# Kernel optimization log

Measured on AMD Instinct MI355X. Metric: run time of the kernel, lower is better.

The kernel has to match this reference:

```python
import jax, jax.numpy as jnp
import numpy as np

N_TREES, N_LEAVES, PATH_LEN, N_NODES, D, B = 10, 16, 5, 31, 256, 4096


def _local_paths():
    # root-to-leaf paths of a full binary tree, depth 4: 31 nodes, 16 leaves, path len 5
    return np.array([[0, 1 + l // 8, 3 + l // 4, 7 + l // 2, 15 + l]
                     for l in range(N_LEAVES)], np.int32)


def setup_inputs() -> dict:
    key = jax.random.key(0)
    k1, k2, k3, k4, k5, k6 = jax.random.split(key, 6)
    # one activated leaf per tree -> multi-hot cross_features (B, N_TREES*N_LEAVES)
    leaf = jax.random.randint(k1, (B, N_TREES), 0, N_LEAVES)
    cross = jnp.zeros((B, N_TREES, N_LEAVES), jnp.float32)
    cross = cross.at[jnp.arange(B)[:, None], jnp.arange(N_TREES)[None, :], leaf].set(1.0)
    cross_features = cross.reshape(B, N_TREES * N_LEAVES)
    # learned params: node embedding table + single-layer LSTM (torch init scale 1/sqrt(D))
    emb = jax.random.normal(k2, (N_TREES * N_NODES, D), jnp.float32) * 0.02
    s = 1.0 / np.sqrt(D)
    W_ih = jax.random.uniform(k3, (4 * D, D), jnp.float32, -s, s)
    W_hh = jax.random.uniform(k4, (4 * D, D), jnp.float32, -s, s)
    b_ih = jax.random.uniform(k5, (4 * D,), jnp.float32, -s, s)
    b_hh = jax.random.uniform(k6, (4 * D,), jnp.float32, -s, s)
    return {"cross_features": cross_features, "emb": emb, "W_ih": W_ih,
            "W_hh": W_hh, "b_ih": b_ih, "b_hh": b_hh}


def reference(cross_features, emb, W_ih, W_hh, b_ih, b_hh):
    # global path node ids per (tree, leaf): [T, L, P]
    gpaths = jnp.asarray(_local_paths())[None, :, :] + \
        (jnp.arange(N_TREES, dtype=jnp.int32) * N_NODES)[:, None, None]
    # activated leaf per tree (exactly one hot per 16-leaf block)
    leaf = jnp.argmax(cross_features.reshape(B, N_TREES, N_LEAVES), axis=-1)  # [B, T]
    node_ids = gpaths[jnp.arange(N_TREES)[None, :], leaf]                     # [B, T, P]
    x = emb[node_ids].reshape(B * N_TREES, PATH_LEN, D)                       # packed paths
    # precompute input projections for all steps: [N, P, 4D]
    xg = jnp.einsum('npd,gd->npg', x, W_ih) + (b_ih + b_hh)

    def step(carry, xt):
        h, c = carry
        g = xt + h @ W_hh.T
        i, f, gg, o = jnp.split(g, 4, axis=-1)  # torch gate order: i, f, g, o
        c = jax.nn.sigmoid(f) * c + jax.nn.sigmoid(i) * jnp.tanh(gg)
        h = jax.nn.sigmoid(o) * jnp.tanh(c)
        return (h, c), None

    n = B * N_TREES
    h0 = jnp.zeros((n, D), x.dtype)
    (h, _), _ = jax.lax.scan(step, (h0, h0), jnp.swapaxes(xg, 0, 1))
    return h.reshape(B, N_TREES, D)
```

## Files before the change

### kernel.cpp

```cpp
#include <hip/hip_runtime.h>

#define NT 10
#define NL 16
#define NN 31
#define DD 256
#define G4 1024
#define NNODES (NT*NN)
#define NPATH (NT*NL)
#define NB 4096

__device__ unsigned g_tf[3][NT][32];

__device__ __forceinline__ float sigf(float x)   { return 1.0f / (1.0f + __expf(-x)); }
__device__ __forceinline__ float tanh_f(float x) { return 2.0f / (1.0f + __expf(-2.0f*x)) - 1.0f; }

__device__ __forceinline__ void co_store(float* p, float v) {
    union { float f; unsigned u; } c; c.f = v;
    __hip_atomic_store((unsigned*)p, c.u, __ATOMIC_RELAXED, __HIP_MEMORY_SCOPE_AGENT);
}

__global__ __launch_bounds__(256) void k_nodeproj(
    const float* __restrict__ emb, const float* __restrict__ Wih,
    const float* __restrict__ bih, const float* __restrict__ bhh,
    float* __restrict__ xg)
{
    __shared__ float smem[20 * 260 + 20 * 4 * 64];
    float4* es4 = (float4*)smem;
    float*  ps  = smem + 20 * 260;

    const int tid = threadIdx.x;
    const int nt  = blockIdx.x & 15;
    const int mt  = blockIdx.x >> 4;
    const int kq  = tid >> 6;
    const int w   = tid & 63;

    const float4* W4 = (const float4*)Wih + (size_t)(nt * 64 + w) * 64 + kq * 16;
    float4 wr[16];
    #pragma unroll
    for (int j = 0; j < 16; ++j) wr[j] = W4[j];

    const float4* emb4 = (const float4*)emb;
    #pragma unroll
    for (int r = 0; r < 5; ++r) {
        int idx = tid + 256 * r;
        int m = idx >> 6, q = idx & 63;
        int n = mt * 20 + m;
        es4[m * 65 + q] = (n < NNODES) ? emb4[(size_t)n * 64 + q]
                                       : make_float4(0.f, 0.f, 0.f, 0.f);
    }
    __syncthreads();

    float acc[20];
    #pragma unroll
    for (int m = 0; m < 20; ++m) acc[m] = 0.f;
    #pragma unroll
    for (int j = 0; j < 16; ++j) {
        float4 wv = wr[j];
        #pragma unroll
        for (int m = 0; m < 20; ++m) {
            float4 h = es4[m * 65 + kq * 16 + j];
            acc[m] = fmaf(wv.x, h.x, fmaf(wv.y, h.y,
                     fmaf(wv.z, h.z, fmaf(wv.w, h.w, acc[m]))));
        }
    }
    #pragma unroll
    for (int m = 0; m < 20; ++m) ps[(m * 4 + kq) * 64 + w] = acc[m];
    __syncthreads();

    const int nl   = tid & 63;
    const int msub = tid >> 6;
    const int j    = nt * 64 + nl;
    const float bsum = bih[j] + bhh[j];
    #pragma unroll
    for (int r = 0; r < 5; ++r) {
        int m = msub * 5 + r;
        int n = mt * 20 + m;
        float s = ps[(m * 4 + 0) * 64 + nl] + ps[(m * 4 + 1) * 64 + nl]
                + ps[(m * 4 + 2) * 64 + nl] + ps[(m * 4 + 3) * 64 + nl];
        if (n < NNODES) xg[(size_t)n * G4 + j] = s + bsum;
    }
}

__global__ __launch_bounds__(256) void k_treesteps(
    const float* __restrict__ xg, const float* __restrict__ Whh,
    float* __restrict__ h1g, float* __restrict__ h2g,
    float* __restrict__ h3g, float* __restrict__ h4g)
{
    __shared__ float hs[8 * DD];
    __shared__ float ps[8 * DD];
    __shared__ float cbuf[2][8 * 16];

    const int tid  = threadIdx.x;
    const int t    = blockIdx.x >> 4;
    const int dt   = blockIdx.x & 15;
    const int kq   = tid >> 6;
    const int w    = tid & 63;
    const int gate = w >> 4;
    const int col  = w & 15;

    const unsigned base = __hip_atomic_load(&g_tf[2][t][0],
        __ATOMIC_RELAXED, __HIP_MEMORY_SCOPE_AGENT);

    const float4* W4 = (const float4*)Whh
        + (size_t)(gate * DD + dt * 16 + col) * 64 + kq * 16;
    float4 wreg[16];
    #pragma unroll
    for (int j = 0; j < 16; ++j) wreg[j] = W4[j];

    float xnv[4][4];
    #pragma unroll
    for (int s = 1; s <= 4; ++s) {
        xnv[s-1][0] = 0.f; xnv[s-1][1] = 0.f;
        xnv[s-1][2] = 0.f; xnv[s-1][3] = 0.f;
        if (tid < (32 << (s - 1))) {
            int node = (1 << s) - 1 + (tid >> 4);
            const float* xn = xg + (size_t)(t * NN + node) * G4 + dt * 16 + (tid & 15);
            xnv[s-1][0] = xn[0];
            xnv[s-1][1] = xn[256];
            xnv[s-1][2] = xn[512];
            xnv[s-1][3] = xn[768];
        }
    }

    {
        const float* xr = xg + (size_t)(t * NN) * G4;
        float r_i = xr[tid], r_g = xr[512 + tid], r_o = xr[768 + tid];
        float c0 = sigf(r_i) * tanh_f(r_g);
        float h0 = sigf(r_o) * tanh_f(c0);
        hs[tid] = h0;
        if ((tid >> 4) == dt) cbuf[0][tid & 15] = c0;
    }
    __syncthreads();

    float* hout[3] = { h1g, h2g, h3g };
    const float* hin[3] = { h1g, h2g, h3g };

    #pragma unroll
    for (int s = 1; s <= 4; ++s) {
        const int L = 1 << (s - 1);

        if (s > 1) {
            if (tid < 64) {
                const unsigned tgt = base + 16u;
                while (__hip_atomic_load(&g_tf[s - 2][t][0],
                        __ATOMIC_RELAXED, __HIP_MEMORY_SCOPE_AGENT) < tgt)
                    __builtin_amdgcn_s_sleep(2);
            }
            __syncthreads();
            const unsigned long long* src =
                (const unsigned long long*)(hin[s - 2] + (size_t)t * L * DD);
            unsigned long long raw[4];
            #pragma unroll
            for (int r = 0; r < L / 2; ++r)
                raw[r] = __hip_atomic_load(src + tid + 256 * r,
                    __ATOMIC_RELAXED, __HIP_MEMORY_SCOPE_AGENT);
            float2* hs2 = (float2*)hs;
            #pragma unroll
            for (int r = 0; r < L / 2; ++r) {
                union { unsigned long long u; float2 f; } cv; cv.u = raw[r];
                hs2[tid + 256 * r] = cv.f;
            }
            __syncthreads();
        }

        const float4* hs4 = (const float4*)hs;
        float acc[8];
        #pragma unroll
        for (int p = 0; p < 8; ++p) acc[p] = 0.f;
        #pragma unroll
        for (int j = 0; j < 16; ++j) {
            float4 wv = wreg[j];
            #pragma unroll
            for (int p = 0; p < L; ++p) {
                float4 h = hs4[p * 64 + kq * 16 + j];
                acc[p] = fmaf(wv.x, h.x, fmaf(wv.y, h.y,
                         fmaf(wv.z, h.z, fmaf(wv.w, h.w, acc[p]))));
            }
        }
        #pragma unroll
        for (int p = 0; p < L; ++p) ps[p * DD + kq * 64 + w] = acc[p];
        __syncthreads();

        if (tid < 32 * L) {
            const int p  = tid >> 5;
            const int c2 = tid & 15;
            const int q  = tid >> 4;
            float g0 = 0.f, g1 = 0.f, g2 = 0.f, g3 = 0.f;
            #pragma unroll
            for (int k = 0; k < 4; ++k) {
                const float* pp = ps + p * DD + k * 64;
                g0 += pp[ 0 + c2]; g1 += pp[16 + c2];
                g2 += pp[32 + c2]; g3 += pp[48 + c2];
            }
            float gi = g0 + xnv[s - 1][0];
            float gf = g1 + xnv[s - 1][1];
            float gg = g2 + xnv[s - 1][2];
            float go = g3 + xnv[s - 1][3];
            float cin = cbuf[(s - 1) & 1][p * 16 + c2];
            float cn  = sigf(gf) * cin + sigf(gi) * tanh_f(gg);
            float hn  = sigf(go) * tanh_f(cn);
            if (s < 4) {
                cbuf[s & 1][q * 16 + c2] = cn;
                co_store(hout[s - 1] + (size_t)(t * 2 * L + q) * DD
                                     + dt * 16 + c2, hn);
            } else {
                h4g[(size_t)(t * NL + q) * DD + dt * 16 + c2] = hn;
            }
        }

        if (s < 4) {
            __syncthreads();
            if (tid == 0)
                __hip_atomic_fetch_add(&g_tf[s - 1][t][0], 1u,
                    __ATOMIC_RELAXED, __HIP_MEMORY_SCOPE_AGENT);
        }
    }
}

__global__ __launch_bounds__(256) void k_scatter(
    const float* __restrict__ cross, const float* __restrict__ htab,
    float* __restrict__ out)
{
    const int tid  = threadIdx.x;
    const int wave = tid >> 6;
    const int lane = tid & 63;
    const int r = blockIdx.x * 4 + wave;
    const int b = r / NT;
    const int t = r - b * NT;

    float v = 0.f;
    if (lane < NL) v = cross[(size_t)b * (NT * NL) + t * NL + lane];
    unsigned long long m = __ballot(v > 0.5f);
    int leaf = m ? (int)__builtin_ctzll(m) : 0;
    int p = t * NL + leaf;

    const float4* h4 = (const float4*)htab;
    float4* o4 = (float4*)out;
    o4[(size_t)r * 64 + lane] = h4[(size_t)p * 64 + lane];
}

extern "C" void kernel_launch(void* const* d_in, const int* in_sizes, int n_in,
                              void* d_out, int out_size, void* d_ws, size_t ws_size,
                              hipStream_t stream)
{
    const float* cross = (const float*)d_in[0];
    const float* emb   = (const float*)d_in[1];
    const float* Wih   = (const float*)d_in[2];
    const float* Whh   = (const float*)d_in[3];
    const float* bih   = (const float*)d_in[4];
    const float* bhh   = (const float*)d_in[5];
    float* out = (float*)d_out;

    float* ws = (float*)d_ws;
    float* xg = ws;
    float* h1 = xg + (size_t)NNODES * G4;
    float* h2 = h1 + 20 * DD;
    float* h3 = h2 + 40 * DD;
    float* h4 = h3 + 80 * DD;

    hipLaunchKernelGGL(k_nodeproj, dim3(256), dim3(256), 0, stream,
                       emb, Wih, bih, bhh, xg);
    hipLaunchKernelGGL(k_treesteps, dim3(160), dim3(256), 0, stream,
                       xg, Whh, h1, h2, h3, h4);
    hipLaunchKernelGGL(k_scatter, dim3(10240), dim3(256), 0, stream,
                       cross, h4, out);
}
```

Baseline: 111.8 us.

## Regroup tree-step LSTM into 4 blocks per tree and batch scatter rows per block

The recurrent tree-step kernel now uses 40 blocks of 512 threads, one per (tree, quarter of hidden dim), instead of 160 blocks of 256 threads. Each thread holds two W_hh rows in registers, and cross-block sync counters become per-quarter flags polled with a wave vote. This cuts the number of blocks that must synchronize through global memory at each step. The scatter kernel now stages 64 rows of cross features in shared memory per block and copies 64 output rows per block, instead of one row per wave. The cost is doubled register pressure in the step kernel and fewer CUs in use.

```diff
diff --git a/kernel.cpp b/kernel.cpp
--- a/kernel.cpp
+++ b/kernel.cpp
@@ -81,54 +81,72 @@
     }
 }
 
-__global__ __launch_bounds__(256) void k_treesteps(
+__global__ __launch_bounds__(512) void k_treesteps(
     const float* __restrict__ xg, const float* __restrict__ Whh,
     float* __restrict__ h1g, float* __restrict__ h2g,
     float* __restrict__ h3g, float* __restrict__ h4g)
 {
     __shared__ float hs[8 * DD];
-    __shared__ float ps[8 * DD];
-    __shared__ float cbuf[2][8 * 16];
-
-    const int tid  = threadIdx.x;
-    const int t    = blockIdx.x >> 4;
-    const int dt   = blockIdx.x & 15;
-    const int kq   = tid >> 6;
-    const int w    = tid & 63;
-    const int gate = w >> 4;
-    const int col  = w & 15;
-
-    const unsigned base = __hip_atomic_load(&g_tf[2][t][0],
-        __ATOMIC_RELAXED, __HIP_MEMORY_SCOPE_AGENT);
-
-    const float4* W4 = (const float4*)Whh
-        + (size_t)(gate * DD + dt * 16 + col) * 64 + kq * 16;
-    float4 wreg[16];
-    #pragma unroll
-    for (int j = 0; j < 16; ++j) wreg[j] = W4[j];
-
-    float xnv[4][4];
+    __shared__ float ps[8 * 4 * DD];
+    __shared__ float cbuf[2][8 * 64];
+
+    const int tid = threadIdx.x;
+    const int t   = blockIdx.x >> 2;
+    const int d4  = blockIdx.x & 3;
+    const int kq  = tid >> 7;
+    const int u   = tid & 127;
+    const int c   = tid & 63;
+    const int q0  = tid >> 6;
+
+    unsigned mybase = 0;
+    if (tid < 4)
+        mybase = __hip_atomic_load(&g_tf[2][t][tid],
+            __ATOMIC_RELAXED, __HIP_MEMORY_SCOPE_AGENT);
+
+    float4 wreg[2][16];
+    #pragma unroll
+    for (int rq = 0; rq < 2; ++rq) {
+        int r    = u + 128 * rq;
+        int grow = (r >> 6) * 256 + d4 * 64 + (r & 63);
+        const float4* Wp = (const float4*)Whh + (size_t)grow * 64 + kq * 16;
+        #pragma unroll
+        for (int j = 0; j < 16; ++j) wreg[rq][j] = Wp[j];
+    }
+
+    float xnv[4][2][4];
     #pragma unroll
     for (int s = 1; s <= 4; ++s) {
-        xnv[s-1][0] = 0.f; xnv[s-1][1] = 0.f;
-        xnv[s-1][2] = 0.f; xnv[s-1][3] = 0.f;
-        if (tid < (32 << (s - 1))) {
-            int node = (1 << s) - 1 + (tid >> 4);
-            const float* xn = xg + (size_t)(t * NN + node) * G4 + dt * 16 + (tid & 15);
-            xnv[s-1][0] = xn[0];
-            xnv[s-1][1] = xn[256];
-            xnv[s-1][2] = xn[512];
-            xnv[s-1][3] = xn[768];
-        }
-    }
-
-    {
+        #pragma unroll
+        for (int h = 0; h < 2; ++h) {
+            xnv[s-1][h][0] = xnv[s-1][h][1] = 0.f;
+            xnv[s-1][h][2] = xnv[s-1][h][3] = 0.f;
+        }
+        int nact = (s == 4) ? 512 : (64 << s);
+        if (tid < nact) {
+            int node = (1 << s) - 1 + q0;
+            const float* xn = xg + (size_t)(t * NN + node) * G4 + d4 * 64 + c;
+            xnv[s-1][0][0] = xn[0];
+            xnv[s-1][0][1] = xn[256];
+            xnv[s-1][0][2] = xn[512];
+            xnv[s-1][0][3] = xn[768];
+        }
+        if (s == 4) {
+            int node = 15 + q0 + 8;
+            const float* xn = xg + (size_t)(t * NN + node) * G4 + d4 * 64 + c;
+            xnv[3][1][0] = xn[0];
+            xnv[3][1][1] = xn[256];
+            xnv[3][1][2] = xn[512];
+            xnv[3][1][3] = xn[768];
+        }
+    }
+
+    if (tid < 256) {
         const float* xr = xg + (size_t)(t * NN) * G4;
         float r_i = xr[tid], r_g = xr[512 + tid], r_o = xr[768 + tid];
         float c0 = sigf(r_i) * tanh_f(r_g);
-        float h0 = sigf(r_o) * tanh_f(c0);
-        hs[tid] = h0;
-        if ((tid >> 4) == dt) cbuf[0][tid & 15] = c0;
+        hs[tid]  = sigf(r_o) * tanh_f(c0);
+        int lc = tid - d4 * 64;
+        if (lc >= 0 && lc < 64) cbuf[0][lc] = c0;
     }
     __syncthreads();
 
@@ -141,77 +159,97 @@
 
         if (s > 1) {
             if (tid < 64) {
-                const unsigned tgt = base + 16u;
-                while (__hip_atomic_load(&g_tf[s - 2][t][0],
-                        __ATOMIC_RELAXED, __HIP_MEMORY_SCOPE_AGENT) < tgt)
-                    __builtin_amdgcn_s_sleep(2);
+                for (;;) {
+                    bool ok = true;
+                    if (tid < 4)
+                        ok = __hip_atomic_load(&g_tf[s - 2][t][tid],
+                                __ATOMIC_RELAXED, __HIP_MEMORY_SCOPE_AGENT)
+                             > mybase;
+                    if (__all(ok)) break;
+                    __builtin_amdgcn_s_sleep(1);
+                }
             }
             __syncthreads();
             const unsigned long long* src =
                 (const unsigned long long*)(hin[s - 2] + (size_t)t * L * DD);
-            unsigned long long raw[4];
-            #pragma unroll
-            for (int r = 0; r < L / 2; ++r)
-                raw[r] = __hip_atomic_load(src + tid + 256 * r,
+            const int n64 = L * 128;
+            unsigned long long raw0 = 0, raw1 = 0;
+            if (tid < n64)
+                raw0 = __hip_atomic_load(src + tid,
+                    __ATOMIC_RELAXED, __HIP_MEMORY_SCOPE_AGENT);
+            if (512 + tid < n64)
+                raw1 = __hip_atomic_load(src + 512 + tid,
                     __ATOMIC_RELAXED, __HIP_MEMORY_SCOPE_AGENT);
             float2* hs2 = (float2*)hs;
-            #pragma unroll
-            for (int r = 0; r < L / 2; ++r) {
-                union { unsigned long long u; float2 f; } cv; cv.u = raw[r];
-                hs2[tid + 256 * r] = cv.f;
+            if (tid < n64) {
+                union { unsigned long long u; float2 f; } cv; cv.u = raw0;
+                hs2[tid] = cv.f;
+            }
+            if (512 + tid < n64) {
+                union { unsigned long long u; float2 f; } cv; cv.u = raw1;
+                hs2[512 + tid] = cv.f;
             }
             __syncthreads();
         }
 
         const float4* hs4 = (const float4*)hs;
-        float acc[8];
-        #pragma unroll
-        for (int p = 0; p < 8; ++p) acc[p] = 0.f;
+        float acc[2][8];
+        #pragma unroll
+        for (int p = 0; p < 8; ++p) { acc[0][p] = 0.f; acc[1][p] = 0.f; }
         #pragma unroll
         for (int j = 0; j < 16; ++j) {
-            float4 wv = wreg[j];
+            float4 w0 = wreg[0][j], w1 = wreg[1][j];
             #pragma unroll
             for (int p = 0; p < L; ++p) {
                 float4 h = hs4[p * 64 + kq * 16 + j];
-                acc[p] = fmaf(wv.x, h.x, fmaf(wv.y, h.y,
-                         fmaf(wv.z, h.z, fmaf(wv.w, h.w, acc[p]))));
-            }
-        }
-        #pragma unroll
-        for (int p = 0; p < L; ++p) ps[p * DD + kq * 64 + w] = acc[p];
+                acc[0][p] = fmaf(w0.x, h.x, fmaf(w0.y, h.y,
+                            fmaf(w0.z, h.z, fmaf(w0.w, h.w, acc[0][p]))));
+                acc[1][p] = fmaf(w1.x, h.x, fmaf(w1.y, h.y,
+                            fmaf(w1.z, h.z, fmaf(w1.w, h.w, acc[1][p]))));
+            }
+        }
+        #pragma unroll
+        for (int p = 0; p < L; ++p) {
+            ps[((p << 2) | kq) * 256 + u]       = acc[0][p];
+            ps[((p << 2) | kq) * 256 + u + 128] = acc[1][p];
+        }
         __syncthreads();
 
-        if (tid < 32 * L) {
-            const int p  = tid >> 5;
-            const int c2 = tid & 15;
-            const int q  = tid >> 4;
-            float g0 = 0.f, g1 = 0.f, g2 = 0.f, g3 = 0.f;
-            #pragma unroll
-            for (int k = 0; k < 4; ++k) {
-                const float* pp = ps + p * DD + k * 64;
-                g0 += pp[ 0 + c2]; g1 += pp[16 + c2];
-                g2 += pp[32 + c2]; g3 += pp[48 + c2];
-            }
-            float gi = g0 + xnv[s - 1][0];
-            float gf = g1 + xnv[s - 1][1];
-            float gg = g2 + xnv[s - 1][2];
-            float go = g3 + xnv[s - 1][3];
-            float cin = cbuf[(s - 1) & 1][p * 16 + c2];
-            float cn  = sigf(gf) * cin + sigf(gi) * tanh_f(gg);
-            float hn  = sigf(go) * tanh_f(cn);
-            if (s < 4) {
-                cbuf[s & 1][q * 16 + c2] = cn;
-                co_store(hout[s - 1] + (size_t)(t * 2 * L + q) * DD
-                                     + dt * 16 + c2, hn);
-            } else {
-                h4g[(size_t)(t * NL + q) * DD + dt * 16 + c2] = hn;
+        const int halves = (s == 4) ? 2 : 1;
+        #pragma unroll
+        for (int hh = 0; hh < halves; ++hh) {
+            int q = q0 + 8 * hh;
+            bool act = (hh == 1) || (tid < (64 << s));
+            if (act) {
+                int p = q >> 1;
+                float g0 = 0.f, g1 = 0.f, g2 = 0.f, g3 = 0.f;
+                #pragma unroll
+                for (int k = 0; k < 4; ++k) {
+                    const float* pp = ps + ((p << 2) | k) * 256;
+                    g0 += pp[c]; g1 += pp[64 + c];
+                    g2 += pp[128 + c]; g3 += pp[192 + c];
+                }
+                float gi = g0 + xnv[s - 1][hh][0];
+                float gf = g1 + xnv[s - 1][hh][1];
+                float gg = g2 + xnv[s - 1][hh][2];
+                float go = g3 + xnv[s - 1][hh][3];
+                float cin = cbuf[(s - 1) & 1][p * 64 + c];
+                float cn  = sigf(gf) * cin + sigf(gi) * tanh_f(gg);
+                float hn  = sigf(go) * tanh_f(cn);
+                if (s < 4) {
+                    cbuf[s & 1][q * 64 + c] = cn;
+                    co_store(hout[s - 1] + (size_t)(t * 2 * L + q) * DD
+                                         + d4 * 64 + c, hn);
+                } else {
+                    h4g[(size_t)(t * NL + q) * DD + d4 * 64 + c] = hn;
+                }
             }
         }
 
         if (s < 4) {
             __syncthreads();
             if (tid == 0)
-                __hip_atomic_fetch_add(&g_tf[s - 1][t][0], 1u,
+                __hip_atomic_fetch_add(&g_tf[s - 1][t][d4], 1u,
                     __ATOMIC_RELAXED, __HIP_MEMORY_SCOPE_AGENT);
         }
     }
@@ -221,22 +259,37 @@
     const float* __restrict__ cross, const float* __restrict__ htab,
     float* __restrict__ out)
 {
-    const int tid  = threadIdx.x;
-    const int wave = tid >> 6;
-    const int lane = tid & 63;
-    const int r = blockIdx.x * 4 + wave;
-    const int b = r / NT;
-    const int t = r - b * NT;
-
-    float v = 0.f;
-    if (lane < NL) v = cross[(size_t)b * (NT * NL) + t * NL + lane];
-    unsigned long long m = __ballot(v > 0.5f);
-    int leaf = m ? (int)__builtin_ctzll(m) : 0;
-    int p = t * NL + leaf;
+    __shared__ float cls[1024];
+    __shared__ int   leafs[64];
+    const int tid = threadIdx.x;
+    const size_t r0 = (size_t)blockIdx.x * 64;
+
+    #pragma unroll
+    for (int k = 0; k < 4; ++k)
+        cls[tid + 256 * k] = cross[r0 * 16 + tid + 256 * k];
+    __syncthreads();
+
+    if (tid < 64) {
+        int leaf = 0;
+        #pragma unroll
+        for (int l = 15; l >= 0; --l)
+            if (cls[tid * 16 + l] > 0.5f) leaf = l;
+        int r = (int)(r0 + (size_t)tid);
+        int b = r / NT;
+        int t = r - b * NT;
+        leafs[tid] = t * 16 + leaf;
+    }
+    __syncthreads();
 
     const float4* h4 = (const float4*)htab;
     float4* o4 = (float4*)out;
-    o4[(size_t)r * 64 + lane] = h4[(size_t)p * 64 + lane];
+    const int lane = tid & 63;
+    const int sub  = tid >> 6;
+    #pragma unroll
+    for (int it = 0; it < 16; ++it) {
+        int rr = it * 4 + sub;
+        o4[(r0 + rr) * 64 + lane] = h4[(size_t)leafs[rr] * 64 + lane];
+    }
 }
 
 extern "C" void kernel_launch(void* const* d_in, const int* in_sizes, int n_in,
@@ -260,8 +313,8 @@
 
     hipLaunchKernelGGL(k_nodeproj, dim3(256), dim3(256), 0, stream,
                        emb, Wih, bih, bhh, xg);
-    hipLaunchKernelGGL(k_treesteps, dim3(160), dim3(256), 0, stream,
+    hipLaunchKernelGGL(k_treesteps, dim3(40), dim3(512), 0, stream,
                        xg, Whh, h1, h2, h3, h4);
-    hipLaunchKernelGGL(k_scatter, dim3(10240), dim3(256), 0, stream,
+    hipLaunchKernelGGL(k_scatter, dim3(640), dim3(256), 0, stream,
                        cross, h4, out);
 }
```

Result: slower. 115.8 us (+3.6%).

## Fuse node projection, tree LSTM steps and leaf scatter into one persistent kernel

Applied to the files above, without the earlier changes.

Merges the three launches into a single kernel whose block ranges play producer/consumer roles, synchronised through generation-counted global flags with release/acquire fences. This removes two launch boundaries and lets the LSTM blocks preload Whh while the projection runs, and lets the scatter blocks decode leaves early. The scatter becomes 256 blocks each handling 160 rows with batched loads, instead of 10240 small blocks. It relies on all 672 blocks being co-resident (launch bounds allow 3 per CU), otherwise the spin-waits can deadlock.

```diff
diff --git a/kernel.cpp b/kernel.cpp
--- a/kernel.cpp
+++ b/kernel.cpp
@@ -9,7 +9,10 @@
 #define NPATH (NT*NL)
 #define NB 4096
 
-__device__ unsigned g_tf[3][NT][32];
+__device__ unsigned g_xgf[16];
+__device__ unsigned g_tf[3][NT][16];
+__device__ unsigned g_h4f[NT];
+__device__ unsigned g_sgen[256];
 
 __device__ __forceinline__ float sigf(float x)   { return 1.0f / (1.0f + __expf(-x)); }
 __device__ __forceinline__ float tanh_f(float x) { return 2.0f / (1.0f + __expf(-2.0f*x)) - 1.0f; }
@@ -18,225 +21,306 @@
     union { float f; unsigned u; } c; c.f = v;
     __hip_atomic_store((unsigned*)p, c.u, __ATOMIC_RELAXED, __HIP_MEMORY_SCOPE_AGENT);
 }
-
-__global__ __launch_bounds__(256) void k_nodeproj(
-    const float* __restrict__ emb, const float* __restrict__ Wih,
-    const float* __restrict__ bih, const float* __restrict__ bhh,
-    float* __restrict__ xg)
-{
-    __shared__ float smem[20 * 260 + 20 * 4 * 64];
-    float4* es4 = (float4*)smem;
-    float*  ps  = smem + 20 * 260;
-
-    const int tid = threadIdx.x;
-    const int nt  = blockIdx.x & 15;
-    const int mt  = blockIdx.x >> 4;
-    const int kq  = tid >> 6;
-    const int w   = tid & 63;
-
-    const float4* W4 = (const float4*)Wih + (size_t)(nt * 64 + w) * 64 + kq * 16;
-    float4 wr[16];
-    #pragma unroll
-    for (int j = 0; j < 16; ++j) wr[j] = W4[j];
-
-    const float4* emb4 = (const float4*)emb;
-    #pragma unroll
-    for (int r = 0; r < 5; ++r) {
-        int idx = tid + 256 * r;
-        int m = idx >> 6, q = idx & 63;
-        int n = mt * 20 + m;
-        es4[m * 65 + q] = (n < NNODES) ? emb4[(size_t)n * 64 + q]
-                                       : make_float4(0.f, 0.f, 0.f, 0.f);
-    }
-    __syncthreads();
-
-    float acc[20];
-    #pragma unroll
-    for (int m = 0; m < 20; ++m) acc[m] = 0.f;
-    #pragma unroll
-    for (int j = 0; j < 16; ++j) {
-        float4 wv = wr[j];
-        #pragma unroll
-        for (int m = 0; m < 20; ++m) {
-            float4 h = es4[m * 65 + kq * 16 + j];
-            acc[m] = fmaf(wv.x, h.x, fmaf(wv.y, h.y,
-                     fmaf(wv.z, h.z, fmaf(wv.w, h.w, acc[m]))));
-        }
-    }
-    #pragma unroll
-    for (int m = 0; m < 20; ++m) ps[(m * 4 + kq) * 64 + w] = acc[m];
-    __syncthreads();
-
-    const int nl   = tid & 63;
-    const int msub = tid >> 6;
-    const int j    = nt * 64 + nl;
-    const float bsum = bih[j] + bhh[j];
-    #pragma unroll
-    for (int r = 0; r < 5; ++r) {
-        int m = msub * 5 + r;
-        int n = mt * 20 + m;
-        float s = ps[(m * 4 + 0) * 64 + nl] + ps[(m * 4 + 1) * 64 + nl]
-                + ps[(m * 4 + 2) * 64 + nl] + ps[(m * 4 + 3) * 64 + nl];
-        if (n < NNODES) xg[(size_t)n * G4 + j] = s + bsum;
-    }
-}
-
-__global__ __launch_bounds__(256) void k_treesteps(
-    const float* __restrict__ xg, const float* __restrict__ Whh,
+__device__ __forceinline__ float co_load(const float* p) {
+    union { unsigned u; float f; } c;
+    c.u = __hip_atomic_load((const unsigned*)p, __ATOMIC_RELAXED, __HIP_MEMORY_SCOPE_AGENT);
+    return c.f;
+}
+__device__ __forceinline__ unsigned long long co_load64(const unsigned long long* p) {
+    return __hip_atomic_load(p, __ATOMIC_RELAXED, __HIP_MEMORY_SCOPE_AGENT);
+}
+__device__ __forceinline__ unsigned flag_load(const unsigned* p) {
+    return __hip_atomic_load(p, __ATOMIC_RELAXED, __HIP_MEMORY_SCOPE_AGENT);
+}
+__device__ __forceinline__ void rel_add(unsigned* p) {
+    __hip_atomic_fetch_add(p, 1u, __ATOMIC_RELEASE, __HIP_MEMORY_SCOPE_AGENT);
+}
+__device__ __forceinline__ void acq_fence() {
+    __builtin_amdgcn_fence(__ATOMIC_ACQUIRE, "agent");
+}
+
+__global__ __launch_bounds__(256, 3) void k_fused(
+    const float* __restrict__ cross, const float* __restrict__ emb,
+    const float* __restrict__ Wih,   const float* __restrict__ Whh,
+    const float* __restrict__ bih,   const float* __restrict__ bhh,
+    float* __restrict__ xg,
     float* __restrict__ h1g, float* __restrict__ h2g,
-    float* __restrict__ h3g, float* __restrict__ h4g)
-{
-    __shared__ float hs[8 * DD];
-    __shared__ float ps[8 * DD];
-    __shared__ float cbuf[2][8 * 16];
-
-    const int tid  = threadIdx.x;
-    const int t    = blockIdx.x >> 4;
-    const int dt   = blockIdx.x & 15;
-    const int kq   = tid >> 6;
-    const int w    = tid & 63;
-    const int gate = w >> 4;
-    const int col  = w & 15;
-
-    const unsigned base = __hip_atomic_load(&g_tf[2][t][0],
-        __ATOMIC_RELAXED, __HIP_MEMORY_SCOPE_AGENT);
-
-    const float4* W4 = (const float4*)Whh
-        + (size_t)(gate * DD + dt * 16 + col) * 64 + kq * 16;
-    float4 wreg[16];
-    #pragma unroll
-    for (int j = 0; j < 16; ++j) wreg[j] = W4[j];
-
-    float xnv[4][4];
-    #pragma unroll
-    for (int s = 1; s <= 4; ++s) {
-        xnv[s-1][0] = 0.f; xnv[s-1][1] = 0.f;
-        xnv[s-1][2] = 0.f; xnv[s-1][3] = 0.f;
-        if (tid < (32 << (s - 1))) {
-            int node = (1 << s) - 1 + (tid >> 4);
-            const float* xn = xg + (size_t)(t * NN + node) * G4 + dt * 16 + (tid & 15);
-            xnv[s-1][0] = xn[0];
-            xnv[s-1][1] = xn[256];
-            xnv[s-1][2] = xn[512];
-            xnv[s-1][3] = xn[768];
-        }
-    }
-
-    {
-        const float* xr = xg + (size_t)(t * NN) * G4;
-        float r_i = xr[tid], r_g = xr[512 + tid], r_o = xr[768 + tid];
-        float c0 = sigf(r_i) * tanh_f(r_g);
-        float h0 = sigf(r_o) * tanh_f(c0);
-        hs[tid] = h0;
-        if ((tid >> 4) == dt) cbuf[0][tid & 15] = c0;
-    }
-    __syncthreads();
-
-    float* hout[3] = { h1g, h2g, h3g };
-    const float* hin[3] = { h1g, h2g, h3g };
-
-    #pragma unroll
-    for (int s = 1; s <= 4; ++s) {
-        const int L = 1 << (s - 1);
-
-        if (s > 1) {
-            if (tid < 64) {
-                const unsigned tgt = base + 16u;
-                while (__hip_atomic_load(&g_tf[s - 2][t][0],
-                        __ATOMIC_RELAXED, __HIP_MEMORY_SCOPE_AGENT) < tgt)
-                    __builtin_amdgcn_s_sleep(2);
-            }
-            __syncthreads();
-            const unsigned long long* src =
-                (const unsigned long long*)(hin[s - 2] + (size_t)t * L * DD);
-            unsigned long long raw[4];
-            #pragma unroll
-            for (int r = 0; r < L / 2; ++r)
-                raw[r] = __hip_atomic_load(src + tid + 256 * r,
-                    __ATOMIC_RELAXED, __HIP_MEMORY_SCOPE_AGENT);
-            float2* hs2 = (float2*)hs;
-            #pragma unroll
-            for (int r = 0; r < L / 2; ++r) {
-                union { unsigned long long u; float2 f; } cv; cv.u = raw[r];
-                hs2[tid + 256 * r] = cv.f;
-            }
-            __syncthreads();
-        }
-
-        const float4* hs4 = (const float4*)hs;
-        float acc[8];
-        #pragma unroll
-        for (int p = 0; p < 8; ++p) acc[p] = 0.f;
-        #pragma unroll
-        for (int j = 0; j < 16; ++j) {
-            float4 wv = wreg[j];
-            #pragma unroll
-            for (int p = 0; p < L; ++p) {
-                float4 h = hs4[p * 64 + kq * 16 + j];
-                acc[p] = fmaf(wv.x, h.x, fmaf(wv.y, h.y,
-                         fmaf(wv.z, h.z, fmaf(wv.w, h.w, acc[p]))));
-            }
-        }
-        #pragma unroll
-        for (int p = 0; p < L; ++p) ps[p * DD + kq * 64 + w] = acc[p];
-        __syncthreads();
-
-        if (tid < 32 * L) {
-            const int p  = tid >> 5;
-            const int c2 = tid & 15;
-            const int q  = tid >> 4;
-            float g0 = 0.f, g1 = 0.f, g2 = 0.f, g3 = 0.f;
-            #pragma unroll
-            for (int k = 0; k < 4; ++k) {
-                const float* pp = ps + p * DD + k * 64;
-                g0 += pp[ 0 + c2]; g1 += pp[16 + c2];
-                g2 += pp[32 + c2]; g3 += pp[48 + c2];
-            }
-            float gi = g0 + xnv[s - 1][0];
-            float gf = g1 + xnv[s - 1][1];
-            float gg = g2 + xnv[s - 1][2];
-            float go = g3 + xnv[s - 1][3];
-            float cin = cbuf[(s - 1) & 1][p * 16 + c2];
-            float cn  = sigf(gf) * cin + sigf(gi) * tanh_f(gg);
-            float hn  = sigf(go) * tanh_f(cn);
-            if (s < 4) {
-                cbuf[s & 1][q * 16 + c2] = cn;
-                co_store(hout[s - 1] + (size_t)(t * 2 * L + q) * DD
-                                     + dt * 16 + c2, hn);
-            } else {
-                h4g[(size_t)(t * NL + q) * DD + dt * 16 + c2] = hn;
-            }
-        }
-
-        if (s < 4) {
-            __syncthreads();
-            if (tid == 0)
-                __hip_atomic_fetch_add(&g_tf[s - 1][t][0], 1u,
-                    __ATOMIC_RELAXED, __HIP_MEMORY_SCOPE_AGENT);
-        }
-    }
-}
-
-__global__ __launch_bounds__(256) void k_scatter(
-    const float* __restrict__ cross, const float* __restrict__ htab,
+    float* __restrict__ h3g, float* __restrict__ h4g,
     float* __restrict__ out)
 {
-    const int tid  = threadIdx.x;
-    const int wave = tid >> 6;
-    const int lane = tid & 63;
-    const int r = blockIdx.x * 4 + wave;
-    const int b = r / NT;
-    const int t = r - b * NT;
-
-    float v = 0.f;
-    if (lane < NL) v = cross[(size_t)b * (NT * NL) + t * NL + lane];
-    unsigned long long m = __ballot(v > 0.5f);
-    int leaf = m ? (int)__builtin_ctzll(m) : 0;
-    int p = t * NL + leaf;
-
-    const float4* h4 = (const float4*)htab;
-    float4* o4 = (float4*)out;
-    o4[(size_t)r * 64 + lane] = h4[(size_t)p * 64 + lane];
+    __shared__ float smem[10320];
+    const int tid = threadIdx.x;
+    const int bid = blockIdx.x;
+
+    if (bid < 160) {
+        float* hs   = smem;
+        float* ps   = smem + 2048;
+        float* cbuf = smem + 4096;
+        float4* hs4 = (float4*)hs;
+
+        const int t    = bid >> 4;
+        const int dt   = bid & 15;
+        const int kq   = tid >> 6;
+        const int w    = tid & 63;
+        const int gate = w >> 4;
+        const int col  = w & 15;
+
+        unsigned G = 0;
+        if (tid < 64) G = flag_load(&g_tf[0][t][dt]);
+
+        const float4* W4 = (const float4*)Whh
+            + (size_t)(gate * DD + dt * 16 + col) * 64 + kq * 16;
+        float4 wreg[16];
+        #pragma unroll
+        for (int j = 0; j < 16; ++j) wreg[j] = W4[j];
+
+        if (tid < 64) {
+            const unsigned tgt = 16u * (G + 1u);
+            for (;;) {
+                bool ok = true;
+                if (tid < 16)
+                    ok = (int)(flag_load(&g_xgf[tid]) - tgt) >= 0;
+                if (__all(ok)) break;
+                __builtin_amdgcn_s_sleep(2);
+            }
+        }
+        __syncthreads();
+        acq_fence();
+
+        float xnv[4][4];
+        #pragma unroll
+        for (int s = 1; s <= 4; ++s) {
+            xnv[s-1][0] = xnv[s-1][1] = xnv[s-1][2] = xnv[s-1][3] = 0.f;
+            if (tid < (32 << (s - 1))) {
+                int node = (1 << s) - 1 + (tid >> 4);
+                const float* xn = xg + (size_t)(t * NN + node) * G4
+                                     + dt * 16 + (tid & 15);
+                xnv[s-1][0] = co_load(xn);
+                xnv[s-1][1] = co_load(xn + 256);
+                xnv[s-1][2] = co_load(xn + 512);
+                xnv[s-1][3] = co_load(xn + 768);
+            }
+        }
+
+        {
+            const float* xr = xg + (size_t)(t * NN) * G4;
+            float r_i = co_load(xr + tid);
+            float r_g = co_load(xr + 512 + tid);
+            float r_o = co_load(xr + 768 + tid);
+            float c0 = sigf(r_i) * tanh_f(r_g);
+            hs[tid]  = sigf(r_o) * tanh_f(c0);
+            if ((tid >> 4) == dt) cbuf[tid & 15] = c0;
+        }
+        __syncthreads();
+
+        float* hout[3] = { h1g, h2g, h3g };
+        const float* hin[3] = { h1g, h2g, h3g };
+
+        #pragma unroll
+        for (int s = 1; s <= 4; ++s) {
+            const int L = 1 << (s - 1);
+
+            if (s > 1) {
+                if (tid < 64) {
+                    const unsigned tgt = G + 1u;
+                    for (;;) {
+                        bool ok = true;
+                        if (tid < 16)
+                            ok = (int)(flag_load(&g_tf[s - 2][t][tid]) - tgt) >= 0;
+                        if (__all(ok)) break;
+                        __builtin_amdgcn_s_sleep(1);
+                    }
+                }
+                __syncthreads();
+                acq_fence();
+                const unsigned long long* src =
+                    (const unsigned long long*)(hin[s - 2] + (size_t)t * L * DD);
+                unsigned long long raw[4];
+                #pragma unroll
+                for (int r = 0; r < L / 2; ++r)
+                    raw[r] = co_load64(src + tid + 256 * r);
+                float2* hs2 = (float2*)hs;
+                #pragma unroll
+                for (int r = 0; r < L / 2; ++r) {
+                    union { unsigned long long u; float2 f; } cv; cv.u = raw[r];
+                    hs2[tid + 256 * r] = cv.f;
+                }
+                __syncthreads();
+            }
+
+            float acc[8];
+            #pragma unroll
+            for (int p = 0; p < 8; ++p) acc[p] = 0.f;
+            #pragma unroll
+            for (int j = 0; j < 16; ++j) {
+                float4 wv = wreg[j];
+                #pragma unroll
+                for (int p = 0; p < L; ++p) {
+                    float4 h = hs4[p * 64 + kq * 16 + j];
+                    acc[p] = fmaf(wv.x, h.x, fmaf(wv.y, h.y,
+                             fmaf(wv.z, h.z, fmaf(wv.w, h.w, acc[p]))));
+                }
+            }
+            #pragma unroll
+            for (int p = 0; p < L; ++p) ps[p * DD + kq * 64 + w] = acc[p];
+            __syncthreads();
+
+            if (tid < 32 * L) {
+                const int p  = tid >> 5;
+                const int c2 = tid & 15;
+                const int q  = tid >> 4;
+                float g0 = 0.f, g1 = 0.f, g2 = 0.f, g3 = 0.f;
+                #pragma unroll
+                for (int k = 0; k < 4; ++k) {
+                    const float* pp = ps + p * DD + k * 64;
+                    g0 += pp[ 0 + c2]; g1 += pp[16 + c2];
+                    g2 += pp[32 + c2]; g3 += pp[48 + c2];
+                }
+                float gi = g0 + xnv[s - 1][0];
+                float gf = g1 + xnv[s - 1][1];
+                float gg = g2 + xnv[s - 1][2];
+                float go = g3 + xnv[s - 1][3];
+                float cin = cbuf[((s - 1) & 1) * 128 + p * 16 + c2];
+                float cn  = sigf(gf) * cin + sigf(gi) * tanh_f(gg);
+                float hn  = sigf(go) * tanh_f(cn);
+                if (s < 4) {
+                    cbuf[(s & 1) * 128 + q * 16 + c2] = cn;
+                    co_store(hout[s - 1] + (size_t)(t * 2 * L + q) * DD
+                                         + dt * 16 + c2, hn);
+                } else {
+                    co_store(h4g + (size_t)(t * NL + q) * DD
+                                 + dt * 16 + c2, hn);
+                }
+            }
+
+            __syncthreads();
+            if (tid == 0) {
+                if (s < 4) rel_add(&g_tf[s - 1][t][dt]);
+                else       rel_add(&g_h4f[t]);
+            }
+        }
+    } else if (bid < 416) {
+        float4* es4 = (float4*)smem;
+        float*  ps  = smem + 5200;
+
+        const int nb  = bid - 160;
+        const int nt  = nb & 15;
+        const int mt  = nb >> 4;
+        const int kq  = tid >> 6;
+        const int w   = tid & 63;
+
+        const float4* W4 = (const float4*)Wih + (size_t)(nt * 64 + w) * 64 + kq * 16;
+        float4 wr[16];
+        #pragma unroll
+        for (int j = 0; j < 16; ++j) wr[j] = W4[j];
+
+        const float4* emb4 = (const float4*)emb;
+        #pragma unroll
+        for (int r = 0; r < 5; ++r) {
+            int idx = tid + 256 * r;
+            int m = idx >> 6, q = idx & 63;
+            int n = mt * 20 + m;
+            es4[m * 65 + q] = (n < NNODES) ? emb4[(size_t)n * 64 + q]
+                                           : make_float4(0.f, 0.f, 0.f, 0.f);
+        }
+        __syncthreads();
+
+        float acc[20];
+        #pragma unroll
+        for (int m = 0; m < 20; ++m) acc[m] = 0.f;
+        #pragma unroll
+        for (int j = 0; j < 16; ++j) {
+            float4 wv = wr[j];
+            #pragma unroll
+            for (int m = 0; m < 20; ++m) {
+                float4 h = es4[m * 65 + kq * 16 + j];
+                acc[m] = fmaf(wv.x, h.x, fmaf(wv.y, h.y,
+                         fmaf(wv.z, h.z, fmaf(wv.w, h.w, acc[m]))));
+            }
+        }
+        #pragma unroll
+        for (int m = 0; m < 20; ++m) ps[(m * 4 + kq) * 64 + w] = acc[m];
+        __syncthreads();
+
+        const int nl   = tid & 63;
+        const int msub = tid >> 6;
+        const int j    = nt * 64 + nl;
+        const float bsum = bih[j] + bhh[j];
+        #pragma unroll
+        for (int r = 0; r < 5; ++r) {
+            int m = msub * 5 + r;
+            int n = mt * 20 + m;
+            float s = ps[(m * 4 + 0) * 64 + nl] + ps[(m * 4 + 1) * 64 + nl]
+                    + ps[(m * 4 + 2) * 64 + nl] + ps[(m * 4 + 3) * 64 + nl];
+            if (n < NNODES) co_store(&xg[(size_t)n * G4 + j], s + bsum);
+        }
+        __syncthreads();
+        if (tid == 0) rel_add(&g_xgf[nt]);
+    } else {
+        float* cls  = smem;
+        int*   leafs = (int*)(smem + 2560);
+
+        const int sb = bid - 416;
+        const size_t r0 = (size_t)sb * 160;
+
+        unsigned G = 0;
+        if (tid < 64) G = flag_load(&g_sgen[sb]);
+        if (tid == 0)
+            __hip_atomic_fetch_add(&g_sgen[sb], 1u,
+                __ATOMIC_RELAXED, __HIP_MEMORY_SCOPE_AGENT);
+
+        #pragma unroll
+        for (int k = 0; k < 10; ++k)
+            cls[tid + 256 * k] = cross[r0 * 16 + tid + 256 * k];
+        __syncthreads();
+        if (tid < 160) {
+            int leaf = 0;
+            #pragma unroll
+            for (int l = 15; l >= 0; --l)
+                if (cls[tid * 16 + l] > 0.5f) leaf = l;
+            int r = (int)(r0 + (size_t)tid);
+            int b = r / NT;
+            int t = r - b * NT;
+            leafs[tid] = t * 16 + leaf;
+        }
+
+        if (tid < 64) {
+            const unsigned tgt = 16u * (G + 1u);
+            for (;;) {
+                bool ok = true;
+                if (tid < NT)
+                    ok = (int)(flag_load(&g_h4f[tid]) - tgt) >= 0;
+                if (__all(ok)) break;
+                __builtin_amdgcn_s_sleep(2);
+            }
+        }
+        __syncthreads();
+        acq_fence();
+
+        const int lane = tid & 63;
+        const int sub  = tid >> 6;
+        float4* o4 = (float4*)out;
+        #pragma unroll
+        for (int batch = 0; batch < 5; ++batch) {
+            unsigned long long a[8], b[8];
+            #pragma unroll
+            for (int i = 0; i < 8; ++i) {
+                int rr = (batch * 8 + i) * 4 + sub;
+                const unsigned long long* hr =
+                    (const unsigned long long*)h4g
+                    + (size_t)leafs[rr] * 128 + lane * 2;
+                a[i] = co_load64(hr);
+                b[i] = co_load64(hr + 1);
+            }
+            #pragma unroll
+            for (int i = 0; i < 8; ++i) {
+                int rr = (batch * 8 + i) * 4 + sub;
+                union { unsigned long long u[2]; float4 f; } cv;
+                cv.u[0] = a[i]; cv.u[1] = b[i];
+                o4[(r0 + rr) * 64 + lane] = cv.f;
+            }
+        }
+    }
 }
 
 extern "C" void kernel_launch(void* const* d_in, const int* in_sizes, int n_in,
@@ -258,10 +342,7 @@
     float* h3 = h2 + 40 * DD;
     float* h4 = h3 + 80 * DD;
 
-    hipLaunchKernelGGL(k_nodeproj, dim3(256), dim3(256), 0, stream,
-                       emb, Wih, bih, bhh, xg);
-    hipLaunchKernelGGL(k_treesteps, dim3(160), dim3(256), 0, stream,
-                       xg, Whh, h1, h2, h3, h4);
-    hipLaunchKernelGGL(k_scatter, dim3(10240), dim3(256), 0, stream,
-                       cross, h4, out);
-}
+    hipLaunchKernelGGL(k_fused, dim3(672), dim3(256), 0, stream,
+                       cross, emb, Wih, Whh, bih, bhh,
+                       xg, h1, h2, h3, h4, out);
+}
```

Result: slower. 156.6 us (+40.1%).

## Use CAS polling with release/acquire flags and batch scatter rows per block

Applied to the files above, without the earlier changes.

The inter-block tree-step barrier now polls from a single thread using an atomic compare-exchange read. The flag increment uses release ordering and readers issue an acquire fence. This aims to cut polling traffic and make cross-block visibility of hidden states explicit. Separately, the scatter kernel now handles 64 rows per block: it stages the one-hot rows in shared memory, finds the leaf with a scalar loop, then copies rows, shrinking the grid from 10240 to 640 blocks. Each CAS poll is a read-modify-write atomic, which can be costlier than a plain load.

```diff
diff --git a/kernel.cpp b/kernel.cpp
--- a/kernel.cpp
+++ b/kernel.cpp
@@ -18,6 +18,21 @@
     union { float f; unsigned u; } c; c.f = v;
     __hip_atomic_store((unsigned*)p, c.u, __ATOMIC_RELAXED, __HIP_MEMORY_SCOPE_AGENT);
 }
+__device__ __forceinline__ unsigned long long co_load64(const unsigned long long* p) {
+    return __hip_atomic_load(p, __ATOMIC_RELAXED, __HIP_MEMORY_SCOPE_AGENT);
+}
+__device__ __forceinline__ unsigned cas_read(unsigned* p) {
+    unsigned exp = 0xFFFFFFFFu;
+    __hip_atomic_compare_exchange_strong(p, &exp, 0xFFFFFFFFu,
+        __ATOMIC_RELAXED, __ATOMIC_RELAXED, __HIP_MEMORY_SCOPE_AGENT);
+    return exp;
+}
+__device__ __forceinline__ void rel_add(unsigned* p) {
+    __hip_atomic_fetch_add(p, 1u, __ATOMIC_RELEASE, __HIP_MEMORY_SCOPE_AGENT);
+}
+__device__ __forceinline__ void acq_fence() {
+    __builtin_amdgcn_fence(__ATOMIC_ACQUIRE, "agent");
+}
 
 __global__ __launch_bounds__(256) void k_nodeproj(
     const float* __restrict__ emb, const float* __restrict__ Wih,
@@ -98,8 +113,8 @@
     const int gate = w >> 4;
     const int col  = w & 15;
 
-    const unsigned base = __hip_atomic_load(&g_tf[2][t][0],
-        __ATOMIC_RELAXED, __HIP_MEMORY_SCOPE_AGENT);
+    unsigned base = 0;
+    if (tid == 0) base = cas_read(&g_tf[2][t][0]);
 
     const float4* W4 = (const float4*)Whh
         + (size_t)(gate * DD + dt * 16 + col) * 64 + kq * 16;
@@ -110,8 +125,7 @@
     float xnv[4][4];
     #pragma unroll
     for (int s = 1; s <= 4; ++s) {
-        xnv[s-1][0] = 0.f; xnv[s-1][1] = 0.f;
-        xnv[s-1][2] = 0.f; xnv[s-1][3] = 0.f;
+        xnv[s-1][0] = xnv[s-1][1] = xnv[s-1][2] = xnv[s-1][3] = 0.f;
         if (tid < (32 << (s - 1))) {
             int node = (1 << s) - 1 + (tid >> 4);
             const float* xn = xg + (size_t)(t * NN + node) * G4 + dt * 16 + (tid & 15);
@@ -126,8 +140,7 @@
         const float* xr = xg + (size_t)(t * NN) * G4;
         float r_i = xr[tid], r_g = xr[512 + tid], r_o = xr[768 + tid];
         float c0 = sigf(r_i) * tanh_f(r_g);
-        float h0 = sigf(r_o) * tanh_f(c0);
-        hs[tid] = h0;
+        hs[tid]  = sigf(r_o) * tanh_f(c0);
         if ((tid >> 4) == dt) cbuf[0][tid & 15] = c0;
     }
     __syncthreads();
@@ -140,20 +153,19 @@
         const int L = 1 << (s - 1);
 
         if (s > 1) {
-            if (tid < 64) {
+            if (tid == 0) {
                 const unsigned tgt = base + 16u;
-                while (__hip_atomic_load(&g_tf[s - 2][t][0],
-                        __ATOMIC_RELAXED, __HIP_MEMORY_SCOPE_AGENT) < tgt)
-                    __builtin_amdgcn_s_sleep(2);
+                while ((int)(cas_read(&g_tf[s - 2][t][0]) - tgt) < 0)
+                    __builtin_amdgcn_s_sleep(4);
             }
             __syncthreads();
+            acq_fence();
             const unsigned long long* src =
                 (const unsigned long long*)(hin[s - 2] + (size_t)t * L * DD);
             unsigned long long raw[4];
             #pragma unroll
             for (int r = 0; r < L / 2; ++r)
-                raw[r] = __hip_atomic_load(src + tid + 256 * r,
-                    __ATOMIC_RELAXED, __HIP_MEMORY_SCOPE_AGENT);
+                raw[r] = co_load64(src + tid + 256 * r);
             float2* hs2 = (float2*)hs;
             #pragma unroll
             for (int r = 0; r < L / 2; ++r) {
@@ -210,9 +222,7 @@
 
         if (s < 4) {
             __syncthreads();
-            if (tid == 0)
-                __hip_atomic_fetch_add(&g_tf[s - 1][t][0], 1u,
-                    __ATOMIC_RELAXED, __HIP_MEMORY_SCOPE_AGENT);
+            if (tid == 0) rel_add(&g_tf[s - 1][t][0]);
         }
     }
 }
@@ -221,22 +231,37 @@
     const float* __restrict__ cross, const float* __restrict__ htab,
     float* __restrict__ out)
 {
-    const int tid  = threadIdx.x;
-    const int wave = tid >> 6;
-    const int lane = tid & 63;
-    const int r = blockIdx.x * 4 + wave;
-    const int b = r / NT;
-    const int t = r - b * NT;
-
-    float v = 0.f;
-    if (lane < NL) v = cross[(size_t)b * (NT * NL) + t * NL + lane];
-    unsigned long long m = __ballot(v > 0.5f);
-    int leaf = m ? (int)__builtin_ctzll(m) : 0;
-    int p = t * NL + leaf;
+    __shared__ float cls[1024];
+    __shared__ int   leafs[64];
+    const int tid = threadIdx.x;
+    const size_t r0 = (size_t)blockIdx.x * 64;
+
+    #pragma unroll
+    for (int k = 0; k < 4; ++k)
+        cls[tid + 256 * k] = cross[r0 * 16 + tid + 256 * k];
+    __syncthreads();
+
+    if (tid < 64) {
+        int leaf = 0;
+        #pragma unroll
+        for (int l = 15; l >= 0; --l)
+            if (cls[tid * 16 + l] > 0.5f) leaf = l;
+        int r = (int)(r0 + (size_t)tid);
+        int b = r / NT;
+        int t = r - b * NT;
+        leafs[tid] = t * 16 + leaf;
+    }
+    __syncthreads();
 
     const float4* h4 = (const float4*)htab;
     float4* o4 = (float4*)out;
-    o4[(size_t)r * 64 + lane] = h4[(size_t)p * 64 + lane];
+    const int lane = tid & 63;
+    const int sub  = tid >> 6;
+    #pragma unroll
+    for (int it = 0; it < 16; ++it) {
+        int rr = it * 4 + sub;
+        o4[(r0 + rr) * 64 + lane] = h4[(size_t)leafs[rr] * 64 + lane];
+    }
 }
 
 extern "C" void kernel_launch(void* const* d_in, const int* in_sizes, int n_in,
@@ -262,6 +287,6 @@
                        emb, Wih, bih, bhh, xg);
     hipLaunchKernelGGL(k_treesteps, dim3(160), dim3(256), 0, stream,
                        xg, Whh, h1, h2, h3, h4);
-    hipLaunchKernelGGL(k_scatter, dim3(10240), dim3(256), 0, stream,
+    hipLaunchKernelGGL(k_scatter, dim3(640), dim3(256), 0, stream,
                        cross, h4, out);
 }
```

Result: slower. 125.0 us (+11.9%).
